# Kernel tuning notes

Measured on AMD Instinct MI355X. Metric: run time of the kernel, lower is better.

The kernel has to match this reference:

```python
import jax, jax.numpy as jnp
import numpy as np

THRESHOLD = 0.5  # decoder threshold (mode='flat')
B, N_SPAN, N_ENT = 4, 1024, 8


def setup_inputs() -> dict:
    key = jax.random.key(0)
    k1, k2, k3 = jax.random.split(key, 3)
    probs = jax.random.uniform(k1, (B, N_SPAN, N_ENT), dtype=jnp.float32)
    starts = jax.random.randint(k2, (B, N_SPAN), 0, 500)
    widths = jax.random.randint(k3, (B, N_SPAN), 0, 11)
    span_indices = jnp.stack([starts, starts + widths], axis=-1).astype(jnp.int64)
    return {"probs": probs, "span_indices": span_indices}


def _decode_one(probs, spans):
    # probs: [n_span, n_ent]; spans: [n_span, 2]
    n_span, n_ent = probs.shape
    N = n_span * n_ent
    scores = probs.reshape(N)                      # flat candidates, span-major
    starts = jnp.repeat(spans[:, 0], n_ent)        # [N]
    ends = jnp.repeat(spans[:, 1], n_ent)          # [N]
    valid = scores > THRESHOLD
    # sort descending by score; below-threshold candidates pushed to the end
    order = jnp.argsort(jnp.where(valid, -scores, jnp.inf))
    s = starts[order]
    e = ends[order]
    sc = jnp.take(scores, order)
    v = valid[order]

    # greedy sequential suppression: a candidate is kept iff it is valid and
    # does not overlap any previously kept (higher-scoring) span ('flat' mode)
    def step(keep, i):
        overlap = ~((e[i] < s) | (e < s[i]))       # [N] pairwise overlap vs all
        conflict = jnp.any(overlap & keep)
        take = v[i] & ~conflict
        keep = keep.at[i].set(take)
        return keep, None

    keep0 = jnp.zeros(N, dtype=bool)
    keep, _ = jax.lax.scan(step, keep0, jnp.arange(N))
    # output: scores of selected candidates (in descending-score order), 0 elsewhere
    return sc * keep.astype(sc.dtype)


def reference(probs, span_indices):
    # [B, n_span*n_ent] selected-candidate scores (greedy flat NMS over spans)
    return jax.vmap(_decode_one)(probs, span_indices)
```

## Files before the change

### kernel.cpp

```cpp
#include <hip/hip_runtime.h>
#include <stdint.h>


#define NSPAN 1024
#define NENT  8
#define NCAND 8192
#define THREADS 1024
#define NWAVE 16

__global__ __launch_bounds__(THREADS)
void decoder_kernel(const float* __restrict__ gprobs,
                    const int* __restrict__ gspans,
                    float* __restrict__ gout) {
    __shared__ uint32_t keyC[NCAND];
    __shared__ uint64_t spanKeyA[NSPAN];
    __shared__ uint64_t spanKeyB[NSPAN];
    __shared__ uint32_t whist[NWAVE*256];
    __shared__ uint32_t spanse[NSPAN];
    __shared__ uint32_t sorted_se[NSPAN];
    __shared__ uint32_t bhist[2048];
    __shared__ uint32_t boffs[2048];
    __shared__ uint32_t barr[NCAND];
    __shared__ uint64_t keptKey[512];
    __shared__ uint32_t wpart[NWAVE], wexc[NWAVE];
    __shared__ uint32_t nvs_sh, keptCnt;

    const int tid = threadIdx.x;
    const int b = blockIdx.x;
    const int W = tid >> 6;
    const int L = tid & 63;

    {
        int s = gspans[(size_t)b * NSPAN * 2 + 2 * tid];
        int e = gspans[(size_t)b * NSPAN * 2 + 2 * tid + 1];
        spanse[tid] = (uint32_t)s | ((uint32_t)e << 16);
    }
    const float* probs = gprobs + (size_t)b * NCAND;
    const float4* p4 = (const float4*)probs;
    float4 pa = p4[tid * 2];
    float4 pb = p4[tid * 2 + 1];
    float pv[8] = {pa.x, pa.y, pa.z, pa.w, pb.x, pb.y, pb.z, pb.w};
    uint32_t k24[8];
    uint64_t skey = ~0ull;
    #pragma unroll
    for (int s = 0; s < 8; ++s) {
        bool valid = pv[s] > 0.5f;
        uint32_t u = ~__float_as_uint(-pv[s]);
        uint32_t k = valid ? (u - 0x407FFFFFu) : 0x00FFFFFFu;
        k24[s] = k;
        keyC[tid * 8 + s] = k;
        uint64_t ck = ((uint64_t)k << 13) | (uint32_t)(tid * 8 + s);
        skey = (ck < skey) ? ck : skey;
    }
    spanKeyA[tid] = skey;
    #pragma unroll
    for (int q = 0; q < 4; ++q) whist[q * 1024 + tid] = 0;
    bhist[tid] = 0; bhist[1024 + tid] = 0;
    if (tid == 0) { nvs_sh = 0; keptCnt = 0; }
    {
        float4 z = make_float4(0.f, 0.f, 0.f, 0.f);
        float4* o4 = (float4*)(gout + (size_t)b * NCAND);
        o4[tid] = z; o4[THREADS + tid] = z;
    }
    __syncthreads();

    for (int p = 0; p < 3; ++p) {
        uint64_t* src = (p & 1) ? spanKeyB : spanKeyA;
        uint64_t* dst = (p & 1) ? spanKeyA : spanKeyB;
        uint64_t kk = src[tid];
        uint32_t d = (uint32_t)(kk >> (13 + 8 * p)) & 255u;
        uint64_t m = ~0ull;
        #pragma unroll
        for (int bb = 0; bb < 8; ++bb) {
            uint64_t bal = __ballot((d >> bb) & 1u);
            m &= ((d >> bb) & 1u) ? bal : ~bal;
        }
        uint32_t lower = __builtin_amdgcn_mbcnt_hi((uint32_t)(m >> 32),
                         __builtin_amdgcn_mbcnt_lo((uint32_t)m, 0u));
        if (lower == 0) whist[W * 256 + d] = (uint32_t)__popcll(m);
        __syncthreads();
        {
            int f0 = 4 * tid;
            uint32_t v0 = whist[((f0 + 0) & 15) * 256 + ((f0 + 0) >> 4)];
            uint32_t v1 = whist[((f0 + 1) & 15) * 256 + ((f0 + 1) >> 4)];
            uint32_t v2 = whist[((f0 + 2) & 15) * 256 + ((f0 + 2) >> 4)];
            uint32_t v3 = whist[((f0 + 3) & 15) * 256 + ((f0 + 3) >> 4)];
            uint32_t t01 = v0 + v1, t012 = t01 + v2, tot = t012 + v3;
            uint32_t x = tot;
            #pragma unroll
            for (int off = 1; off < 64; off <<= 1) {
                uint32_t y = __shfl_up(x, off, 64);
                if (L >= off) x += y;
            }
            if (L == 63) wpart[W] = x;
            __syncthreads();
            if (tid < 16) {
                uint32_t v = wpart[tid], xx = v;
                #pragma unroll
                for (int off = 1; off < 16; off <<= 1) {
                    uint32_t y = __shfl_up(xx, off, 64);
                    if (tid >= off) xx += y;
                }
                wexc[tid] = xx - v;
            }
            __syncthreads();
            uint32_t ex = wexc[W] + (x - tot);
            whist[((f0 + 0) & 15) * 256 + ((f0 + 0) >> 4)] = ex;
            whist[((f0 + 1) & 15) * 256 + ((f0 + 1) >> 4)] = ex + v0;
            whist[((f0 + 2) & 15) * 256 + ((f0 + 2) >> 4)] = ex + t01;
            whist[((f0 + 3) & 15) * 256 + ((f0 + 3) >> 4)] = ex + t012;
        }
        __syncthreads();
        dst[whist[W * 256 + d] + lower] = kk;
        __syncthreads();
        if (p < 2) {
            #pragma unroll
            for (int q = 0; q < 4; ++q) whist[q * 1024 + tid] = 0;
            __syncthreads();
        }
    }

    {
        uint64_t sk = spanKeyB[tid];
        uint32_t sidx = (uint32_t)sk & 8191u;
        sorted_se[tid] = spanse[sidx >> 3];
        bool vs = (uint32_t)(sk >> 13) < 0x800000u;
        uint64_t bv = __ballot(vs);
        if (L == 0) atomicAdd((unsigned int*)&nvs_sh, (unsigned int)__popcll(bv));
    }
    #pragma unroll
    for (int s = 0; s < 8; ++s) {
        uint32_t k = k24[s];
        if (k < 0x800000u) atomicAdd((unsigned int*)&bhist[k >> 12], 1u);
    }
    __syncthreads();

    {
        int f0 = 2 * tid;
        uint32_t v0 = bhist[f0], v1 = bhist[f0 + 1];
        uint32_t tot = v0 + v1, x = tot;
        #pragma unroll
        for (int off = 1; off < 64; off <<= 1) {
            uint32_t y = __shfl_up(x, off, 64);
            if (L >= off) x += y;
        }
        if (L == 63) wpart[W] = x;
        __syncthreads();
        if (tid < 16) {
            uint32_t v = wpart[tid], xx = v;
            #pragma unroll
            for (int off = 1; off < 16; off <<= 1) {
                uint32_t y = __shfl_up(xx, off, 64);
                if (tid >= off) xx += y;
            }
            wexc[tid] = xx - v;
        }
        __syncthreads();
        uint32_t ex = wexc[W] + (x - tot);
        boffs[f0] = ex; boffs[f0 + 1] = ex + v0;
    }
    __syncthreads();
    whist[tid] = boffs[tid];
    whist[1024 + tid] = boffs[1024 + tid];
    __syncthreads();

    const uint32_t nvs = nvs_sh;
    if (W == 0) {
        uint64_t Bm[8] = {0, 0, 0, 0, 0, 0, 0, 0};
        uint32_t K = 0;
        int nchunk = ((int)nvs + 63) >> 6;
        for (int c = 0; c < nchunk; ++c) {
            int i = c * 64 + L;
            uint64_t sk = spanKeyB[i];
            uint32_t se = sorted_se[i];
            bool valid = (uint32_t)(sk >> 13) < 0x800000u;

            int s = (int)(se & 0xFFFFu);
            int e = (int)(se >> 16);
            int w0 = s >> 6, w1 = e >> 6;
            uint64_t m0 = (~0ull) << (s & 63);
            uint64_t m1 = (~0ull) >> (63 - (e & 63));
            if (w0 == w1) { m0 &= m1; m1 = 0ull; }

            uint64_t bs0 = 0, bs1 = 0;
            #pragma unroll
            for (int w = 0; w < 8; ++w) {
                bs0 = (w0 == w) ? Bm[w] : bs0;
                bs1 = (w1 == w) ? Bm[w] : bs1;
            }
            uint64_t conf = (m0 & bs0) | (m1 & bs1);
            bool undecided = valid;

            while (true) {
                uint64_t cand = __ballot(undecided && conf == 0ull);
                if (cand == 0ull) break;
                int jl = __ffsll((unsigned long long)cand) - 1;
                if (undecided && L <= jl) {
                    undecided = false;
                    if (L == jl) keptKey[K] = sk;
                }
                K++;
                uint32_t sew = (uint32_t)__builtin_amdgcn_readlane((int)se, jl);
                uint32_t ss = sew & 0xFFFFu, ee = sew >> 16;
                int sw0 = (int)(ss >> 6), sw1 = (int)(ee >> 6);
                uint64_t sm0 = (~0ull) << (ss & 63u);
                uint64_t sm1 = (~0ull) >> (63u - (ee & 63u));
                if (sw0 == sw1) { sm0 &= sm1; sm1 = 0ull; }
                #pragma unroll
                for (int w = 0; w < 8; ++w) {
                    uint64_t add = ((sw0 == w) ? sm0 : 0ull) | ((sw1 == w) ? sm1 : 0ull);
                    Bm[w] |= add;
                }
                uint64_t d0 = ((w0 == sw0) ? sm0 : 0ull) | ((w0 == sw1) ? sm1 : 0ull);
                uint64_t d1 = ((w1 == sw0) ? sm0 : 0ull) | ((w1 == sw1) ? sm1 : 0ull);
                conf |= (m0 & d0) | (m1 & d1);
            }
        }
        if (L == 0) keptCnt = K;
    } else {
        for (int i = tid - 64; i < NCAND; i += THREADS - 64) {
            uint32_t k = keyC[i];
            if (k < 0x800000u) {
                uint32_t pos = atomicAdd((unsigned int*)&whist[k >> 12], 1u);
                barr[pos] = ((k & 0xFFFu) << 13) | (uint32_t)i;
            }
        }
    }
    __syncthreads();

    if (tid < (int)keptCnt) {
        uint64_t kk = keptKey[tid];
        uint32_t idx = (uint32_t)kk & 8191u;
        uint32_t kv = (uint32_t)(kk >> 13) & 0xFFFFFFu;
        uint32_t bkt = kv >> 12;
        uint32_t lo = ((kv & 0xFFFu) << 13) | idx;
        uint32_t beg = boffs[bkt];
        uint32_t cnt = bhist[bkt];
        uint32_t r = beg;
        for (uint32_t j = 0; j < cnt; ++j) r += (barr[beg + j] < lo) ? 1u : 0u;
        uint32_t u = kv + 0x407FFFFFu;
        float score = -__uint_as_float(~u);
        gout[(size_t)b * NCAND + r] = score;
    }
}

extern "C" void kernel_launch(void* const* d_in, const int* in_sizes, int n_in,
                              void* d_out, int out_size, void* d_ws, size_t ws_size,
                              hipStream_t stream) {
    const float* probs = (const float*)d_in[0];
    const int* spans = (const int*)d_in[1];
    float* out = (float*)d_out;
    int B = in_sizes[0] / NCAND;
    decoder_kernel<<<dim3(B), dim3(THREADS), 0, stream>>>(probs, spans, out);
}
```

Before: 99.52 us.

## Replace span radix sort with combined counting-sort bucket scatter and in-bucket ranking

Result: faster. 96.40 us (-3.1%).

```diff
diff --git a/kernel.cpp b/kernel.cpp
--- a/kernel.cpp
+++ b/kernel.cpp
@@ -7,20 +7,18 @@
 #define NCAND 8192
 #define THREADS 1024
 #define NWAVE 16
+#define NCNT 3072
+#define SCATMAX (NSPAN + NCAND)
 
 __global__ __launch_bounds__(THREADS)
 void decoder_kernel(const float* __restrict__ gprobs,
                     const int* __restrict__ gspans,
                     float* __restrict__ gout) {
-    __shared__ uint32_t keyC[NCAND];
-    __shared__ uint64_t spanKeyA[NSPAN];
-    __shared__ uint64_t spanKeyB[NSPAN];
-    __shared__ uint32_t whist[NWAVE*256];
-    __shared__ uint32_t spanse[NSPAN];
-    __shared__ uint32_t sorted_se[NSPAN];
-    __shared__ uint32_t bhist[2048];
-    __shared__ uint32_t boffs[2048];
-    __shared__ uint32_t barr[NCAND];
+    __shared__ uint32_t cnt_[NCNT];
+    __shared__ uint32_t cur_[NCNT];
+    __shared__ uint32_t scat[SCATMAX];
+    __shared__ uint64_t sortedCand[NSPAN];
+    __shared__ uint32_t sortedSE[NSPAN];
     __shared__ uint64_t keptKey[512];
     __shared__ uint32_t wpart[NWAVE], wexc[NWAVE];
     __shared__ uint32_t nvs_sh, keptCnt;
@@ -30,115 +28,48 @@
     const int W = tid >> 6;
     const int L = tid & 63;
 
+    cnt_[tid] = 0; cnt_[1024 + tid] = 0; cnt_[2048 + tid] = 0;
+    if (tid == 0) keptCnt = 0;
+
+    int s0 = gspans[(size_t)b * NSPAN * 2 + 2 * tid];
+    int e0 = gspans[(size_t)b * NSPAN * 2 + 2 * tid + 1];
+    const uint32_t myse = (uint32_t)s0 | ((uint32_t)e0 << 16);
+
+    const float4* p4 = (const float4*)(gprobs + (size_t)b * NCAND);
+    float4 pa = p4[tid * 2], pb = p4[tid * 2 + 1];
+    float pv[8] = {pa.x, pa.y, pa.z, pa.w, pb.x, pb.y, pb.z, pb.w};
+
     {
-        int s = gspans[(size_t)b * NSPAN * 2 + 2 * tid];
-        int e = gspans[(size_t)b * NSPAN * 2 + 2 * tid + 1];
-        spanse[tid] = (uint32_t)s | ((uint32_t)e << 16);
-    }
-    const float* probs = gprobs + (size_t)b * NCAND;
-    const float4* p4 = (const float4*)probs;
-    float4 pa = p4[tid * 2];
-    float4 pb = p4[tid * 2 + 1];
-    float pv[8] = {pa.x, pa.y, pa.z, pa.w, pb.x, pb.y, pb.z, pb.w};
+        float4 z = make_float4(0.f, 0.f, 0.f, 0.f);
+        float4* o4 = (float4*)(gout + (size_t)b * NCAND);
+        o4[tid] = z; o4[THREADS + tid] = z;
+    }
+
     uint32_t k24[8];
     uint64_t skey = ~0ull;
     #pragma unroll
     for (int s = 0; s < 8; ++s) {
         bool valid = pv[s] > 0.5f;
         uint32_t u = ~__float_as_uint(-pv[s]);
-        uint32_t k = valid ? (u - 0x407FFFFFu) : 0x00FFFFFFu;
+        uint32_t k = valid ? (u - 0x407FFFFFu) : 0xFFFFFFu;
         k24[s] = k;
-        keyC[tid * 8 + s] = k;
         uint64_t ck = ((uint64_t)k << 13) | (uint32_t)(tid * 8 + s);
         skey = (ck < skey) ? ck : skey;
     }
-    spanKeyA[tid] = skey;
+    const uint32_t sk24 = (uint32_t)(skey >> 13);
+    const bool spanValid = sk24 < 0x800000u;
+    __syncthreads();
+
+    if (spanValid) atomicAdd(&cnt_[sk24 >> 13], 1u);
     #pragma unroll
-    for (int q = 0; q < 4; ++q) whist[q * 1024 + tid] = 0;
-    bhist[tid] = 0; bhist[1024 + tid] = 0;
-    if (tid == 0) { nvs_sh = 0; keptCnt = 0; }
+    for (int s = 0; s < 8; ++s)
+        if (k24[s] < 0x800000u) atomicAdd(&cnt_[1024 + (k24[s] >> 12)], 1u);
+    __syncthreads();
+
     {
-        float4 z = make_float4(0.f, 0.f, 0.f, 0.f);
-        float4* o4 = (float4*)(gout + (size_t)b * NCAND);
-        o4[tid] = z; o4[THREADS + tid] = z;
-    }
-    __syncthreads();
-
-    for (int p = 0; p < 3; ++p) {
-        uint64_t* src = (p & 1) ? spanKeyB : spanKeyA;
-        uint64_t* dst = (p & 1) ? spanKeyA : spanKeyB;
-        uint64_t kk = src[tid];
-        uint32_t d = (uint32_t)(kk >> (13 + 8 * p)) & 255u;
-        uint64_t m = ~0ull;
-        #pragma unroll
-        for (int bb = 0; bb < 8; ++bb) {
-            uint64_t bal = __ballot((d >> bb) & 1u);
-            m &= ((d >> bb) & 1u) ? bal : ~bal;
-        }
-        uint32_t lower = __builtin_amdgcn_mbcnt_hi((uint32_t)(m >> 32),
-                         __builtin_amdgcn_mbcnt_lo((uint32_t)m, 0u));
-        if (lower == 0) whist[W * 256 + d] = (uint32_t)__popcll(m);
-        __syncthreads();
-        {
-            int f0 = 4 * tid;
-            uint32_t v0 = whist[((f0 + 0) & 15) * 256 + ((f0 + 0) >> 4)];
-            uint32_t v1 = whist[((f0 + 1) & 15) * 256 + ((f0 + 1) >> 4)];
-            uint32_t v2 = whist[((f0 + 2) & 15) * 256 + ((f0 + 2) >> 4)];
-            uint32_t v3 = whist[((f0 + 3) & 15) * 256 + ((f0 + 3) >> 4)];
-            uint32_t t01 = v0 + v1, t012 = t01 + v2, tot = t012 + v3;
-            uint32_t x = tot;
-            #pragma unroll
-            for (int off = 1; off < 64; off <<= 1) {
-                uint32_t y = __shfl_up(x, off, 64);
-                if (L >= off) x += y;
-            }
-            if (L == 63) wpart[W] = x;
-            __syncthreads();
-            if (tid < 16) {
-                uint32_t v = wpart[tid], xx = v;
-                #pragma unroll
-                for (int off = 1; off < 16; off <<= 1) {
-                    uint32_t y = __shfl_up(xx, off, 64);
-                    if (tid >= off) xx += y;
-                }
-                wexc[tid] = xx - v;
-            }
-            __syncthreads();
-            uint32_t ex = wexc[W] + (x - tot);
-            whist[((f0 + 0) & 15) * 256 + ((f0 + 0) >> 4)] = ex;
-            whist[((f0 + 1) & 15) * 256 + ((f0 + 1) >> 4)] = ex + v0;
-            whist[((f0 + 2) & 15) * 256 + ((f0 + 2) >> 4)] = ex + t01;
-            whist[((f0 + 3) & 15) * 256 + ((f0 + 3) >> 4)] = ex + t012;
-        }
-        __syncthreads();
-        dst[whist[W * 256 + d] + lower] = kk;
-        __syncthreads();
-        if (p < 2) {
-            #pragma unroll
-            for (int q = 0; q < 4; ++q) whist[q * 1024 + tid] = 0;
-            __syncthreads();
-        }
-    }
-
-    {
-        uint64_t sk = spanKeyB[tid];
-        uint32_t sidx = (uint32_t)sk & 8191u;
-        sorted_se[tid] = spanse[sidx >> 3];
-        bool vs = (uint32_t)(sk >> 13) < 0x800000u;
-        uint64_t bv = __ballot(vs);
-        if (L == 0) atomicAdd((unsigned int*)&nvs_sh, (unsigned int)__popcll(bv));
-    }
-    #pragma unroll
-    for (int s = 0; s < 8; ++s) {
-        uint32_t k = k24[s];
-        if (k < 0x800000u) atomicAdd((unsigned int*)&bhist[k >> 12], 1u);
-    }
-    __syncthreads();
-
-    {
-        int f0 = 2 * tid;
-        uint32_t v0 = bhist[f0], v1 = bhist[f0 + 1];
-        uint32_t tot = v0 + v1, x = tot;
+        uint32_t v0 = cnt_[3 * tid], v1 = cnt_[3 * tid + 1], v2 = cnt_[3 * tid + 2];
+        uint32_t t01 = v0 + v1, tot = t01 + v2;
+        uint32_t x = tot;
         #pragma unroll
         for (int off = 1; off < 64; off <<= 1) {
             uint32_t y = __shfl_up(x, off, 64);
@@ -157,23 +88,52 @@
         }
         __syncthreads();
         uint32_t ex = wexc[W] + (x - tot);
-        boffs[f0] = ex; boffs[f0 + 1] = ex + v0;
-    }
-    __syncthreads();
-    whist[tid] = boffs[tid];
-    whist[1024 + tid] = boffs[1024 + tid];
+        cur_[3 * tid] = ex;
+        cur_[3 * tid + 1] = ex + v0;
+        cur_[3 * tid + 2] = ex + t01;
+        if (3 * tid <= 1024 && 1024 < 3 * tid + 3) {
+            uint32_t nv = (1024 == 3 * tid) ? ex : ((1024 == 3 * tid + 1) ? ex + v0 : ex + t01);
+            nvs_sh = nv;
+        }
+    }
+    __syncthreads();
+
+    if (spanValid) {
+        uint32_t pos = atomicAdd(&cur_[sk24 >> 13], 1u);
+        scat[pos] = ((sk24 & 0x1FFFu) << 10) | (uint32_t)tid;
+    }
+    #pragma unroll
+    for (int s = 0; s < 8; ++s) {
+        uint32_t k = k24[s];
+        if (k < 0x800000u) {
+            uint32_t pos = atomicAdd(&cur_[1024 + (k >> 12)], 1u);
+            scat[pos] = ((k & 0xFFFu) << 13) | (uint32_t)(tid * 8 + s);
+        }
+    }
     __syncthreads();
 
     const uint32_t nvs = nvs_sh;
+    if (spanValid) {
+        uint32_t bkt = sk24 >> 13;
+        uint32_t c = cnt_[bkt];
+        uint32_t beg = cur_[bkt] - c;
+        uint32_t mykey = ((sk24 & 0x1FFFu) << 10) | (uint32_t)tid;
+        uint32_t r = 0;
+        for (uint32_t j = 0; j < c; ++j) r += (scat[beg + j] < mykey) ? 1u : 0u;
+        sortedCand[beg + r] = skey;
+        sortedSE[beg + r] = myse;
+    }
+    __syncthreads();
+
     if (W == 0) {
         uint64_t Bm[8] = {0, 0, 0, 0, 0, 0, 0, 0};
         uint32_t K = 0;
         int nchunk = ((int)nvs + 63) >> 6;
         for (int c = 0; c < nchunk; ++c) {
             int i = c * 64 + L;
-            uint64_t sk = spanKeyB[i];
-            uint32_t se = sorted_se[i];
-            bool valid = (uint32_t)(sk >> 13) < 0x800000u;
+            bool valid = i < (int)nvs;
+            uint64_t sk = sortedCand[i];
+            uint32_t se = sortedSE[i];
 
             int s = (int)(se & 0xFFFFu);
             int e = (int)(se >> 16);
@@ -217,30 +177,22 @@
             }
         }
         if (L == 0) keptCnt = K;
-    } else {
-        for (int i = tid - 64; i < NCAND; i += THREADS - 64) {
-            uint32_t k = keyC[i];
-            if (k < 0x800000u) {
-                uint32_t pos = atomicAdd((unsigned int*)&whist[k >> 12], 1u);
-                barr[pos] = ((k & 0xFFFu) << 13) | (uint32_t)i;
-            }
-        }
     }
     __syncthreads();
 
     if (tid < (int)keptCnt) {
         uint64_t kk = keptKey[tid];
         uint32_t idx = (uint32_t)kk & 8191u;
-        uint32_t kv = (uint32_t)(kk >> 13) & 0xFFFFFFu;
-        uint32_t bkt = kv >> 12;
-        uint32_t lo = ((kv & 0xFFFu) << 13) | idx;
-        uint32_t beg = boffs[bkt];
-        uint32_t cnt = bhist[bkt];
-        uint32_t r = beg;
-        for (uint32_t j = 0; j < cnt; ++j) r += (barr[beg + j] < lo) ? 1u : 0u;
-        uint32_t u = kv + 0x407FFFFFu;
-        float score = -__uint_as_float(~u);
-        gout[(size_t)b * NCAND + r] = score;
+        uint32_t kv = (uint32_t)(kk >> 13);
+        uint32_t bkt = 1024 + (kv >> 12);
+        uint32_t c = cnt_[bkt];
+        uint32_t beg = cur_[bkt] - c;
+        uint32_t mykey = ((kv & 0xFFFu) << 13) | idx;
+        uint32_t r = 0;
+        for (uint32_t j = 0; j < c; ++j) r += (scat[beg + j] < mykey) ? 1u : 0u;
+        uint32_t outpos = (beg - nvs) + r;
+        float score = -__uint_as_float(~(kv + 0x407FFFFFu));
+        gout[(size_t)b * NCAND + outpos] = score;
     }
 }
 
```
